# Kernel optimization log

Measured on AMD Instinct MI355X. Metric: run time of the kernel, lower is better.

Reference implementation:

```python
import jax, jax.numpy as jnp
import numpy as np

B, T, M, D = 8, 512, 16, 128
P, H = 256, 8
E = P // H


def setup_inputs() -> dict:
    key = jax.random.key(0)
    ks = jax.random.split(key, 5)
    inp = jax.random.normal(ks[0], (B, T, M, D), dtype=jnp.float32)
    mask = jax.random.randint(ks[1], (B, T, M), 0, 2).astype(bool)
    sc = 1.0 / np.sqrt(D).astype(np.float32)
    Wq = jax.random.normal(ks[2], (D, P), dtype=jnp.float32) * sc
    Wk = jax.random.normal(ks[3], (D, P), dtype=jnp.float32) * sc
    Wv = jax.random.normal(ks[4], (D, P), dtype=jnp.float32) * sc
    z = jnp.zeros((P,), dtype=jnp.float32)
    return {"inp": inp, "mask": mask, "Wq": Wq, "bq": z, "Wk": Wk, "bk": z, "Wv": Wv, "bv": z}


def _split_heads(x):
    # (b, t, m, h*e) -> (b, m, h, t, e)
    b, t, m, _ = x.shape
    return x.reshape(b, t, m, H, E).transpose(0, 2, 3, 1, 4)


def reference(inp, mask, Wq, bq, Wk, bk, Wv, bv):
    q = _split_heads(inp @ Wq + bq)
    k = _split_heads(inp @ Wk + bk)
    v = _split_heads(inp @ Wv + bv)
    # scores over time axis per (batch, modality, head): (b, m, h, t, t)
    score = jnp.einsum('bmhte,bmhse->bmhts', q, k) / np.float32(np.sqrt(E))
    kmask = mask.transpose(0, 2, 1)[:, :, None, None, :]  # (b, m, 1, 1, t)
    score = jnp.where(kmask, score, -jnp.inf)
    weight = jax.nn.softmax(score, axis=-1)
    weight = jnp.where(kmask, weight, jnp.zeros((), weight.dtype))
    out = jnp.einsum('bmhts,bmhse->bmhte', weight, v)
    b, m, h, t, e = out.shape
    return out.transpose(0, 3, 1, 2, 4).reshape(b, t, m, h * e)
```

## Files before the change

kernel.cpp:

```cpp
#include <hip/hip_runtime.h>
#include <stdint.h>

#define B_ 8
#define T_ 512
#define M_ 16
#define D_ 128
#define P_ 256
#define H_ 8
#define E_ 32

typedef __attribute__((ext_vector_type(8))) short  short8;
typedef __attribute__((ext_vector_type(4))) short  short4v;
typedef __attribute__((ext_vector_type(4))) float  float4v;
typedef __attribute__((ext_vector_type(2))) unsigned int uint2v;
typedef __attribute__((ext_vector_type(4))) unsigned int uint4v;
typedef __attribute__((ext_vector_type(2))) __bf16 bf16x2;

#define MFMA32(a,b,c) __builtin_amdgcn_mfma_f32_16x16x32_bf16(a,b,c,0,0,0)
#define EXP2F(x) __builtin_amdgcn_exp2f(x)

#define C2 0.2550332772062413f

static __device__ __forceinline__ unsigned short f2bf(float x){
  unsigned int u = __builtin_bit_cast(unsigned int, x);
  u += 0x7FFFu + ((u >> 16) & 1u);
  return (unsigned short)(u >> 16);
}

static __device__ __forceinline__ unsigned int pk2(float a, float b){
  bf16x2 h; h[0] = (__bf16)a; h[1] = (__bf16)b;
  return __builtin_bit_cast(unsigned int, h);
}

static __device__ __forceinline__ short4v pack4(float4v v){
  uint2v u; u.x = pk2(v[0], v[1]); u.y = pk2(v[2], v[3]);
  return __builtin_bit_cast(short4v, u);
}

static __device__ __forceinline__ short8 pack8(float4v a, float4v b){
  uint4v u; u.x = pk2(a[0],a[1]); u.y = pk2(a[2],a[3]);
  u.z = pk2(b[0],b[1]); u.w = pk2(b[2],b[3]);
  return __builtin_bit_cast(short8, u);
}

static __device__ __forceinline__ short8 cat44(short4v lo, short4v hi){
  short8 r;
  r[0]=lo[0]; r[1]=lo[1]; r[2]=lo[2]; r[3]=lo[3];
  r[4]=hi[0]; r[5]=hi[1]; r[6]=hi[2]; r[7]=hi[3];
  return r;
}

__global__ void prep(const float* __restrict__ Wq, const float* __restrict__ Wk,
                     const float* __restrict__ Wv, const int* __restrict__ mask,
                     uint16_t* __restrict__ WT, float* __restrict__ maskf){
  int idx = blockIdx.x*256 + threadIdx.x;
  if (idx < 3*P_*D_){
    int d = idx & (D_-1);
    int p = (idx >> 7) & (P_-1);
    int z = idx >> 15;
    int col = p;
    if (z < 2){
      int w = p & 31;
      int e = ((w>>2)&3)*8 + ((w>>4)&1)*4 + (w&3);
      col = (p & ~31) | e;
    }
    const float* W = (z==0) ? Wq : (z==1) ? Wk : Wv;
    float sc = (z==0) ? C2 : 1.0f;
    WT[idx] = f2bf(W[d*P_ + col] * sc);
  } else {
    int j = idx - 3*P_*D_;
    int s = j & (T_-1);
    int bm = j >> 9;
    int b = bm >> 4, m = bm & (M_-1);
    maskf[j] = mask[(b*T_ + s)*M_ + m] ? 0.0f : -1e30f;
  }
}

__global__ __launch_bounds__(512, 4) void attn_fused(
    const float* __restrict__ inp, const uint16_t* __restrict__ WT,
    const float* __restrict__ bq, const float* __restrict__ bk,
    const float* __restrict__ bv, const float* __restrict__ maskf,
    float* __restrict__ out){
  __shared__ __align__(16) uint16_t Kb[T_*E_];
  __shared__ __align__(16) uint16_t Vt[E_*T_];

  const int bx = blockIdx.x;
  const int h = bx >> 7, bm = bx & 127;
  const int b = bm >> 4, m = bm & 15;
  const int tid = threadIdx.x;
  const int wave = tid >> 6, lane = tid & 63;
  const int q4 = lane >> 4, c = lane & 15;
  const int t0 = wave*64;

  short8 af[4][4];
  for (int tj=0; tj<4; tj++){
    const float* src = inp + (size_t)((b*T_ + t0 + tj*16 + c)*M_ + m)*D_;
    for (int kc=0; kc<4; kc++){
      float4v x0 = *(const float4v*)(src + kc*32 + q4*8);
      float4v x1 = *(const float4v*)(src + kc*32 + q4*8 + 4);
      af[tj][kc] = pack8(x0, x1);
    }
  }

  const uint16_t* WQ = WT                       + (size_t)(h*E_)*D_;
  const uint16_t* WK = WT + (size_t)1*P_*D_     + (size_t)(h*E_)*D_;
  const uint16_t* WV = WT + (size_t)2*P_*D_     + (size_t)(h*E_)*D_;
  float4v zf = {0.f,0.f,0.f,0.f};

  for (int eh=0; eh<2; eh++){
    float4v ka[4]; for (int j=0;j<4;j++) ka[j]=zf;
    for (int kc=0; kc<4; kc++){
      short8 w = *(const short8*)(WK + (size_t)(eh*16 + c)*D_ + kc*32 + q4*8);
      for (int sj=0; sj<4; sj++) ka[sj] = MFMA32(w, af[sj][kc], ka[sj]);
    }
    float4v bk4 = *(const float4v*)(bk + h*E_ + q4*8 + eh*4);
    for (int sj=0; sj<4; sj++){
      int s = t0 + sj*16 + c;
      short4v kv = pack4(ka[sj] + bk4);
      *(short4v*)(Kb + s*32 + ((q4 ^ (s&3))<<3) + eh*4) = kv;
    }
  }
  for (int eh=0; eh<2; eh++){
    float4v va[4]; for (int j=0;j<4;j++) va[j]=zf;
    for (int kc=0; kc<4; kc++){
      short8 w = *(const short8*)(WV + (size_t)(eh*16 + c)*D_ + kc*32 + q4*8);
      for (int sj=0; sj<4; sj++) va[sj] = MFMA32(w, af[sj][kc], va[sj]);
    }
    float4v bv4 = *(const float4v*)(bv + h*E_ + eh*16 + q4*4);
    for (int sj=0; sj<4; sj++){
      int s = t0 + sj*16 + c;
      short4v vv = pack4(va[sj] + bv4);
      for (int r=0; r<4; r++){
        int e = eh*16 + q4*4 + r;
        Vt[e*T_ + ((((s>>2) + e) & 127)*4) + (s&3)] = (uint16_t)vv[r];
      }
    }
  }
  short8 q8[4];
  {
    short4v qtmp[4][2];
    for (int eh=0; eh<2; eh++){
      float4v qa[4]; for (int j=0;j<4;j++) qa[j]=zf;
      for (int kc=0; kc<4; kc++){
        short8 w = *(const short8*)(WQ + (size_t)(eh*16 + c)*D_ + kc*32 + q4*8);
        for (int tj=0; tj<4; tj++) qa[tj] = MFMA32(w, af[tj][kc], qa[tj]);
      }
      float4v bq4 = *(const float4v*)(bq + h*E_ + q4*8 + eh*4);
      bq4 *= C2;
      for (int tj=0; tj<4; tj++) qtmp[tj][eh] = pack4(qa[tj] + bq4);
    }
    for (int tj=0; tj<4; tj++) q8[tj] = cat44(qtmp[tj][0], qtmp[tj][1]);
  }
  __syncthreads();

  float4v O[4][2], L4[4];
  for (int i=0;i<4;i++){ O[i][0]=zf; O[i][1]=zf; L4[i]=zf; }
  const short one_bf = (short)0x3F80;
  short8 ones8;
  for (int i=0;i<8;i++) ones8[i] = one_bf;
  const float* mrow = maskf + (size_t)bm*T_;

  for (int sb=0; sb<16; sb++){
    const int sq = sb*32;
    float4v mm0 = *(const float4v*)(mrow + sq + q4*4);
    float4v mm1 = *(const float4v*)(mrow + sq + 16 + q4*4);
    const int srow0 = sq + c, srow1 = sq + 16 + c;
    short8 kb8_0 = *(const short8*)(Kb + srow0*32 + ((q4 ^ (srow0&3))<<3));
    short8 kb8_1 = *(const short8*)(Kb + srow1*32 + ((q4 ^ (srow1&3))<<3));
    const int u0 = sb*8 + q4, u1 = u0 + 4;
    short4v vA0 = *(const short4v*)(Vt + (size_t)c*T_      + ((u0 + c     ) & 127)*4);
    short4v vA1 = *(const short4v*)(Vt + (size_t)c*T_      + ((u1 + c     ) & 127)*4);
    short4v vB0 = *(const short4v*)(Vt + (size_t)(16+c)*T_ + ((u0 + 16 + c) & 127)*4);
    short4v vB1 = *(const short4v*)(Vt + (size_t)(16+c)*T_ + ((u1 + 16 + c) & 127)*4);
    short8 V8_0 = cat44(vA0, vA1);
    short8 V8_1 = cat44(vB0, vB1);
    for (int tj=0; tj<4; tj++){
      float4v st0 = MFMA32(kb8_0, q8[tj], mm0);
      float4v st1 = MFMA32(kb8_1, q8[tj], mm1);
      float4v p0, p1;
      p0[0] = EXP2F(st0[0]); p0[1] = EXP2F(st0[1]);
      p0[2] = EXP2F(st0[2]); p0[3] = EXP2F(st0[3]);
      p1[0] = EXP2F(st1[0]); p1[1] = EXP2F(st1[1]);
      p1[2] = EXP2F(st1[2]); p1[3] = EXP2F(st1[3]);
      short8 A8 = pack8(p0, p1);
      O[tj][0] = MFMA32(A8, V8_0, O[tj][0]);
      O[tj][1] = MFMA32(A8, V8_1, O[tj][1]);
      L4[tj]   = MFMA32(A8, ones8, L4[tj]);
    }
  }

  for (int ti=0; ti<4; ti++){
    float4v linv;
    for (int r=0; r<4; r++) linv[r] = __builtin_amdgcn_rcpf(L4[ti][r]);
    for (int ej=0; ej<2; ej++){
      float4v v = O[ti][ej] * linv;
      for (int r=0; r<4; r++){
        int t = t0 + ti*16 + q4*4 + r;
        out[(size_t)((b*T_ + t)*M_ + m)*P_ + h*E_ + ej*16 + c] = v[r];
      }
    }
  }
}

extern "C" void kernel_launch(void* const* d_in, const int* in_sizes, int n_in,
                              void* d_out, int out_size, void* d_ws, size_t ws_size,
                              hipStream_t stream){
  const float* inp = (const float*)d_in[0];
  const int*   msk = (const int*)  d_in[1];
  const float* Wq  = (const float*)d_in[2];
  const float* bq  = (const float*)d_in[3];
  const float* Wk  = (const float*)d_in[4];
  const float* bk  = (const float*)d_in[5];
  const float* Wv  = (const float*)d_in[6];
  const float* bv  = (const float*)d_in[7];
  float* out = (float*)d_out;

  uint16_t* WT    = (uint16_t*)d_ws;
  float*    maskf = (float*)((char*)d_ws + 196608);

  prep<<<dim3(640), dim3(256), 0, stream>>>(Wq, Wk, Wv, msk, WT, maskf);
  attn_fused<<<dim3(1024), dim3(512), 0, stream>>>(inp, WT, bq, bk, bv, maskf, out);
}
```

Before: 176.0 us.

## Fuse mask conversion into attention kernel, coalesce weight prep reads, add setprio

```diff
diff --git a/kernel.cpp b/kernel.cpp
--- a/kernel.cpp
+++ b/kernel.cpp
@@ -51,38 +51,30 @@
 }
 
 __global__ void prep(const float* __restrict__ Wq, const float* __restrict__ Wk,
-                     const float* __restrict__ Wv, const int* __restrict__ mask,
-                     uint16_t* __restrict__ WT, float* __restrict__ maskf){
+                     const float* __restrict__ Wv, uint16_t* __restrict__ WT){
   int idx = blockIdx.x*256 + threadIdx.x;
-  if (idx < 3*P_*D_){
-    int d = idx & (D_-1);
-    int p = (idx >> 7) & (P_-1);
-    int z = idx >> 15;
-    int col = p;
-    if (z < 2){
-      int w = p & 31;
-      int e = ((w>>2)&3)*8 + ((w>>4)&1)*4 + (w&3);
-      col = (p & ~31) | e;
-    }
-    const float* W = (z==0) ? Wq : (z==1) ? Wk : Wv;
-    float sc = (z==0) ? C2 : 1.0f;
-    WT[idx] = f2bf(W[d*P_ + col] * sc);
-  } else {
-    int j = idx - 3*P_*D_;
-    int s = j & (T_-1);
-    int bm = j >> 9;
-    int b = bm >> 4, m = bm & (M_-1);
-    maskf[j] = mask[(b*T_ + s)*M_ + m] ? 0.0f : -1e30f;
-  }
+  int p = idx & (P_-1);
+  int d = (idx >> 8) & (D_-1);
+  int z = idx >> 15;
+  int col = p;
+  if (z < 2){
+    int w = p & 31;
+    int e = ((w>>2)&3)*8 + ((w>>4)&1)*4 + (w&3);
+    col = (p & ~31) | e;
+  }
+  const float* W = (z==0) ? Wq : (z==1) ? Wk : Wv;
+  float sc = (z==0) ? C2 : 1.0f;
+  WT[(z<<15) + (p<<7) + d] = f2bf(W[d*P_ + col] * sc);
 }
 
 __global__ __launch_bounds__(512, 4) void attn_fused(
     const float* __restrict__ inp, const uint16_t* __restrict__ WT,
     const float* __restrict__ bq, const float* __restrict__ bk,
-    const float* __restrict__ bv, const float* __restrict__ maskf,
+    const float* __restrict__ bv, const int* __restrict__ mask,
     float* __restrict__ out){
   __shared__ __align__(16) uint16_t Kb[T_*E_];
   __shared__ __align__(16) uint16_t Vt[E_*T_];
+  __shared__ __align__(16) float    Mrow[T_];
 
   const int bx = blockIdx.x;
   const int h = bx >> 7, bm = bx & 127;
@@ -91,6 +83,11 @@
   const int wave = tid >> 6, lane = tid & 63;
   const int q4 = lane >> 4, c = lane & 15;
   const int t0 = wave*64;
+
+  {
+    int mv = mask[((size_t)(b*T_ + tid))*M_ + m];
+    Mrow[tid] = mv ? 0.0f : -1e30f;
+  }
 
   short8 af[4][4];
   for (int tj=0; tj<4; tj++){
@@ -158,12 +155,11 @@
   const short one_bf = (short)0x3F80;
   short8 ones8;
   for (int i=0;i<8;i++) ones8[i] = one_bf;
-  const float* mrow = maskf + (size_t)bm*T_;
 
   for (int sb=0; sb<16; sb++){
     const int sq = sb*32;
-    float4v mm0 = *(const float4v*)(mrow + sq + q4*4);
-    float4v mm1 = *(const float4v*)(mrow + sq + 16 + q4*4);
+    float4v mm0 = *(const float4v*)(Mrow + sq + q4*4);
+    float4v mm1 = *(const float4v*)(Mrow + sq + 16 + q4*4);
     const int srow0 = sq + c, srow1 = sq + 16 + c;
     short8 kb8_0 = *(const short8*)(Kb + srow0*32 + ((q4 ^ (srow0&3))<<3));
     short8 kb8_1 = *(const short8*)(Kb + srow1*32 + ((q4 ^ (srow1&3))<<3));
@@ -174,6 +170,7 @@
     short4v vB1 = *(const short4v*)(Vt + (size_t)(16+c)*T_ + ((u1 + 16 + c) & 127)*4);
     short8 V8_0 = cat44(vA0, vA1);
     short8 V8_1 = cat44(vB0, vB1);
+    __builtin_amdgcn_s_setprio(1);
     for (int tj=0; tj<4; tj++){
       float4v st0 = MFMA32(kb8_0, q8[tj], mm0);
       float4v st1 = MFMA32(kb8_1, q8[tj], mm1);
@@ -187,6 +184,7 @@
       O[tj][1] = MFMA32(A8, V8_1, O[tj][1]);
       L4[tj]   = MFMA32(A8, ones8, L4[tj]);
     }
+    __builtin_amdgcn_s_setprio(0);
   }
 
   for (int ti=0; ti<4; ti++){
@@ -215,9 +213,8 @@
   const float* bv  = (const float*)d_in[7];
   float* out = (float*)d_out;
 
-  uint16_t* WT    = (uint16_t*)d_ws;
-  float*    maskf = (float*)((char*)d_ws + 196608);
-
-  prep<<<dim3(640), dim3(256), 0, stream>>>(Wq, Wk, Wv, msk, WT, maskf);
-  attn_fused<<<dim3(1024), dim3(512), 0, stream>>>(inp, WT, bq, bk, bv, maskf, out);
-}
+  uint16_t* WT = (uint16_t*)d_ws;
+
+  prep<<<dim3(384), dim3(256), 0, stream>>>(Wq, Wk, Wv, WT);
+  attn_fused<<<dim3(1024), dim3(512), 0, stream>>>(inp, WT, bq, bk, bv, msk, out);
+}
```

Result: slower. 180.9 us (+2.8%).
